# Optimization experiments

Hardware: AMD Instinct MI355X
Metric: run time of the kernel (lower is better)

The kernel has to match this reference:

```python
import jax, jax.numpy as jnp
import numpy as np

BASE_TEMP = 0.07
CLASS_TEMPS = jnp.array([0.08, 0.05, 0.10], dtype=jnp.float32)  # idx 0,1,2
EPS = 1e-08


def setup_inputs() -> dict:
    key = jax.random.key(0)
    k1, k2 = jax.random.split(key)
    B, D = 8192, 128
    embeddings = jax.random.normal(k1, (B, D), dtype=jnp.float32)
    labels = jax.random.randint(k2, (B,), 0, 3, dtype=jnp.int64)
    return {"embeddings": embeddings, "labels": labels}


def reference(embeddings, labels):
    B = embeddings.shape[0]
    # per-row temperature from the row's class label
    temps = CLASS_TEMPS[labels]  # [B]
    sim = jnp.matmul(embeddings, embeddings.T)  # [B, B]
    logits = sim / temps[:, None]
    # subtract detached row max (stability, gradient-stopped as in .detach())
    logits = logits - jax.lax.stop_gradient(jnp.max(logits, axis=1, keepdims=True))
    # denominator includes the self term (original sums exp over all j)
    log_prob = logits - jnp.log(jnp.sum(jnp.exp(logits), axis=1, keepdims=True) + EPS)
    # positives: same label, excluding self
    pos_mask = (labels[:, None] == labels[None, :]).astype(jnp.float32)
    pos_mask = pos_mask * (1.0 - jnp.eye(B, dtype=jnp.float32))
    pos_count = jnp.sum(pos_mask, axis=1)  # [B]
    valid = pos_count > 0
    loss_i = -(BASE_TEMP / temps) * jnp.sum(pos_mask * log_prob, axis=1) / (pos_count + EPS)
    n_valid = jnp.sum(valid.astype(jnp.float32))
    total = jnp.sum(jnp.where(valid, loss_i, 0.0))
    return jnp.where(n_valid > 0, total / jnp.maximum(n_valid, 1.0), 0.0)
```

## Files before the change

### kernel.cpp

```cpp
#include <hip/hip_runtime.h>
#include <hip/hip_bf16.h>


#define B_ROWS 8192
#define D_DIM 128
#define NSPLIT 16
#define JRANGE (B_ROWS / NSPLIT)
#define NSTEPS (JRANGE / 32)
#define BASE_TEMP 0.07f
#define LOG2E 1.4426950408889634f
#define LN2 0.6931471805599453f
#define FIX_SCALE 1048576.0f

typedef __bf16 bf16x8 __attribute__((ext_vector_type(8)));
typedef __bf16 bf16x4 __attribute__((ext_vector_type(4)));
typedef float floatx16 __attribute__((ext_vector_type(16)));
typedef unsigned long long u64;

__device__ __forceinline__ float class_invtemp(int lbl) {
    return (lbl == 0) ? 12.5f : ((lbl == 1) ? 20.0f : 10.0f);
}

__device__ __forceinline__ u64 fix64(float v) {
    return (u64)(long long)llrintf(v * FIX_SCALE);
}

__device__ __forceinline__ void load_lds16(const __bf16* g, __bf16* l) {
    __builtin_amdgcn_global_load_lds(
        (const __attribute__((address_space(1))) void*)g,
        (__attribute__((address_space(3))) void*)l,
        16, 0, 0);
}

__global__ __launch_bounds__(256) void k0_prep(
        const float* __restrict__ E, const int* __restrict__ labels,
        __bf16* __restrict__ Ebf, __bf16* __restrict__ Ebs,
        float* __restrict__ nrm,
        float* __restrict__ Spart ,
        int* __restrict__ cntpart ) {
    const int blk = blockIdx.x;
    const int tid = threadIdx.x;
    const int row0 = blk * 32;

    __shared__ float4 red[3][256];
    __shared__ int scnt[3];
    if (tid < 3) scnt[tid] = 0;

    float4 cls0 = {0.f, 0.f, 0.f, 0.f};
    float4 cls1 = {0.f, 0.f, 0.f, 0.f};
    float4 cls2 = {0.f, 0.f, 0.f, 0.f};

    const float4* src = reinterpret_cast<const float4*>(E + (size_t)row0 * D_DIM);
    #pragma unroll
    for (int p = 0; p < 4; ++p) {
        int idx = p * 256 + tid;
        float4 v = src[idx];
        int r = idx >> 5, k4 = idx & 31;
        int R = row0 + r;
        int lab = labels[R];
        float sc = class_invtemp(lab) * LOG2E;
        int T = R >> 5;
        int l = (R & 31) + ((k4 >> 1) & 1) * 32;
        int c = k4 >> 2;
        size_t dst = (size_t)T * 4096 + c * 512 + l * 8 + (k4 & 1) * 4;
        bf16x4 o  = { (__bf16)v.x, (__bf16)v.y, (__bf16)v.z, (__bf16)v.w };
        bf16x4 os = { (__bf16)(v.x * sc), (__bf16)(v.y * sc),
                      (__bf16)(v.z * sc), (__bf16)(v.w * sc) };
        *reinterpret_cast<bf16x4*>(Ebf + dst) = o;
        *reinterpret_cast<bf16x4*>(Ebs + dst) = os;
        float s = v.x * v.x + v.y * v.y + v.z * v.z + v.w * v.w;
        s += __shfl_xor(s, 1);  s += __shfl_xor(s, 2);  s += __shfl_xor(s, 4);
        s += __shfl_xor(s, 8);  s += __shfl_xor(s, 16);
        if ((tid & 31) == 0) nrm[R] = s;
        if (lab == 0) { cls0.x += v.x; cls0.y += v.y; cls0.z += v.z; cls0.w += v.w; }
        else if (lab == 1) { cls1.x += v.x; cls1.y += v.y; cls1.z += v.z; cls1.w += v.w; }
        else { cls2.x += v.x; cls2.y += v.y; cls2.z += v.z; cls2.w += v.w; }
    }
    red[0][tid] = cls0;
    red[1][tid] = cls1;
    red[2][tid] = cls2;
    if (tid < 32) atomicAdd(&scnt[labels[row0 + tid]], 1);
    __syncthreads();

    if (tid < 128) {
        const int k4 = tid >> 2, comp = tid & 3;
        const float* rf = reinterpret_cast<const float*>(red);
        #pragma unroll
        for (int c = 0; c < 3; ++c) {
            float a = 0.f;
            #pragma unroll
            for (int w = 0; w < 8; ++w)
                a += rf[(c * 256 + k4 + 32 * w) * 4 + comp];
            Spart[((size_t)blk * 3 + c) * 128 + tid] = a;
        }
    }
    if (tid < 3) cntpart[blk * 4 + tid] = scnt[tid];
}

__global__ __launch_bounds__(256) void k2_stats(
        const __bf16* __restrict__ Ebf, const __bf16* __restrict__ Ebs,
        const int* __restrict__ labels, const float* __restrict__ nrm,
        float* __restrict__ part ,
        const float* __restrict__ Spart, const int* __restrict__ cntpart,
        float* __restrict__ S , float* __restrict__ counts ,
        u64* __restrict__ lossfix, u64* __restrict__ validfix,
        unsigned int* __restrict__ done) {
    __shared__ __bf16 Ab[3][4096];

    const int tid = threadIdx.x;
    const int lane = tid & 63;
    const int wave = tid >> 6;
    const int itile = blockIdx.x;
    const int split = blockIdx.y;
    const int col = lane & 31;
    const int icol = itile * 128 + wave * 32 + col;

    const float negm = -class_invtemp(labels[icol]) * LOG2E * nrm[icol];

    const int iT = itile * 4 + wave;
    const __bf16* bbase = Ebs + (size_t)iT * 4096 + lane * 8;
    bf16x8 Bf[8];
    #pragma unroll
    for (int c = 0; c < 8; ++c)
        Bf[c] = *reinterpret_cast<const bf16x8*>(bbase + c * 512);

    floatx16 init0;
    #pragma unroll
    for (int r = 0; r < 16; ++r) init0[r] = negm;

    const __bf16* abase = Ebf + (size_t)split * NSTEPS * 4096;
    const int woff = wave * 1024 + lane * 8;

    load_lds16(abase + woff,              &Ab[0][wave * 1024]);
    load_lds16(abase + woff + 512,        &Ab[0][wave * 1024 + 512]);
    load_lds16(abase + 4096 + woff,       &Ab[1][wave * 1024]);
    load_lds16(abase + 4096 + woff + 512, &Ab[1][wave * 1024 + 512]);

    float Zacc[4];
    #pragma unroll
    for (int q = 0; q < 4; ++q) Zacc[q] = 0.f;

    #pragma unroll 1
    for (int s = 0; s < NSTEPS; ++s) {
        if (s < NSTEPS - 1) {
            asm volatile("s_waitcnt vmcnt(2)" ::: "memory");
        } else {
            asm volatile("s_waitcnt vmcnt(0)" ::: "memory");
        }
        __builtin_amdgcn_s_barrier();
        __builtin_amdgcn_sched_barrier(0);

        if (s + 2 < NSTEPS) {
            const __bf16* g = abase + (size_t)(s + 2) * 4096 + woff;
            __bf16* l = &Ab[(s + 2) % 3][wave * 1024];
            load_lds16(g, l);
            load_lds16(g + 512, l + 512);
        }

        const __bf16* abuf = &Ab[s % 3][0];
        bf16x8 A[8];
        #pragma unroll
        for (int c = 0; c < 8; ++c)
            A[c] = *reinterpret_cast<const bf16x8*>(abuf + c * 512 + lane * 8);

        floatx16 a1;
        #pragma unroll
        for (int r = 0; r < 16; ++r) a1[r] = 0.f;
        floatx16 a0 = __builtin_amdgcn_mfma_f32_32x32x16_bf16(A[0], Bf[0], init0, 0, 0, 0);
        a1 = __builtin_amdgcn_mfma_f32_32x32x16_bf16(A[4], Bf[4], a1, 0, 0, 0);
        a0 = __builtin_amdgcn_mfma_f32_32x32x16_bf16(A[1], Bf[1], a0, 0, 0, 0);
        a1 = __builtin_amdgcn_mfma_f32_32x32x16_bf16(A[5], Bf[5], a1, 0, 0, 0);
        a0 = __builtin_amdgcn_mfma_f32_32x32x16_bf16(A[2], Bf[2], a0, 0, 0, 0);
        a1 = __builtin_amdgcn_mfma_f32_32x32x16_bf16(A[6], Bf[6], a1, 0, 0, 0);
        a0 = __builtin_amdgcn_mfma_f32_32x32x16_bf16(A[3], Bf[3], a0, 0, 0, 0);
        a1 = __builtin_amdgcn_mfma_f32_32x32x16_bf16(A[7], Bf[7], a1, 0, 0, 0);

        #pragma unroll
        for (int q = 0; q < 4; ++q) {
            Zacc[q] += (__builtin_amdgcn_exp2f(a0[4 * q]     + a1[4 * q])
                      + __builtin_amdgcn_exp2f(a0[4 * q + 1] + a1[4 * q + 1]))
                     + (__builtin_amdgcn_exp2f(a0[4 * q + 2] + a1[4 * q + 2])
                      + __builtin_amdgcn_exp2f(a0[4 * q + 3] + a1[4 * q + 3]));
        }
    }

    float Zt = (Zacc[0] + Zacc[1]) + (Zacc[2] + Zacc[3]);
    Zt += __shfl_xor(Zt, 32);
    if (lane < 32)
        part[(size_t)split * B_ROWS + icol] = Zt;

    if (split == 0) {
        if (itile < 3 && tid < 128) {
            float a = 0.f;
            #pragma unroll 8
            for (int g = 0; g < 256; ++g)
                a += Spart[((size_t)g * 3 + itile) * 128 + tid];
            S[itile * 128 + tid] = a;
        } else if (itile == 3 && tid < 3) {
            int a = 0;
            #pragma unroll 8
            for (int g = 0; g < 256; ++g) a += cntpart[g * 4 + tid];
            counts[tid] = (float)a;
        } else if (itile == 4 && tid == 0) {
            *lossfix = 0ull;
            *validfix = 0ull;
            *done = 0u;
        }
    }
}

__global__ __launch_bounds__(256) void k3_rowloss(
        const float* __restrict__ E, const int* __restrict__ labels,
        const float* __restrict__ S, const float* __restrict__ counts,
        const float* __restrict__ nrm, const float* __restrict__ part,
        u64* __restrict__ lossfix, u64* __restrict__ validfix,
        unsigned int* __restrict__ done, float* __restrict__ out) {
    __shared__ float sS[384];
    const int tid = threadIdx.x;
    if (tid < 128) {
        sS[tid]       = S[tid];
        sS[128 + tid] = S[128 + tid];
        sS[256 + tid] = S[256 + tid];
    }
    __syncthreads();

    const int r = tid >> 3, g = tid & 7;
    const int i = blockIdx.x * 32 + r;
    const int lab = labels[i];
    const float invt = class_invtemp(lab);

    const float4* er = reinterpret_cast<const float4*>(E + (size_t)i * D_DIM);
    const float4* sr = reinterpret_cast<const float4*>(&sS[lab * 128]);
    float dotS = 0.f;
    #pragma unroll
    for (int q = 0; q < 4; ++q) {
        float4 v = er[g * 4 + q];
        float4 s = sr[g * 4 + q];
        dotS += v.x * s.x + v.y * s.y + v.z * s.z + v.w * s.w;
    }
    float Zp = 0.f;
    #pragma unroll
    for (int p = 0; p < NSPLIT / 8; ++p)
        Zp += part[(size_t)(g + p * 8) * B_ROWS + i];

    #pragma unroll
    for (int off = 1; off < 8; off <<= 1) {
        dotS += __shfl_xor(dotS, off);
        Zp   += __shfl_xor(Zp, off);
    }

    float loss = 0.f;
    int valid = 0;
    if (g == 0) {
        const float nr = nrm[i];
        const float C = counts[lab] - 1.0f;
        const float lse = invt * nr + LN2 * __builtin_amdgcn_logf(Zp);
        const float P_nat = invt * (dotS - nr);
        if (C > 0.f) {
            loss = -(BASE_TEMP * invt) * (P_nat - C * lse) / (C + 1e-8f);
            valid = 1;
        }
    }
    loss += __shfl_down(loss, 8);   valid += __shfl_down(valid, 8);
    loss += __shfl_down(loss, 16);  valid += __shfl_down(valid, 16);
    loss += __shfl_down(loss, 32);  valid += __shfl_down(valid, 32);

    __shared__ float rl[4];
    __shared__ int rv[4];
    if ((tid & 63) == 0) { rl[tid >> 6] = loss; rv[tid >> 6] = valid; }
    __syncthreads();
    if (tid == 0) {
        float bt = (rl[0] + rl[1]) + (rl[2] + rl[3]);
        int bv = (rv[0] + rv[1]) + (rv[2] + rv[3]);
        atomicAdd(lossfix, fix64(bt));
        atomicAdd(validfix, (u64)bv);
        __threadfence();
        unsigned int t = atomicAdd(done, 1u);
        if (t == gridDim.x - 1) {
            u64 L = atomicAdd(lossfix, 0ull);
            u64 V = atomicAdd(validfix, 0ull);
            double T = (double)(long long)L * (1.0 / (double)FIX_SCALE);
            double N = (double)(long long)V;
            out[0] = (N > 0.0) ? (float)(T / fmax(N, 1.0)) : 0.f;
        }
    }
}

extern "C" void kernel_launch(void* const* d_in, const int* in_sizes, int n_in,
                              void* d_out, int out_size, void* d_ws, size_t ws_size,
                              hipStream_t stream) {
    const float* E = (const float*)d_in[0];
    const int* labels = (const int*)d_in[1];
    float* out = (float*)d_out;
    char* ws = (char*)d_ws;

    const size_t OFF_EBF   = 0;
    const size_t OFF_EBS   = (size_t)2 << 20;
    const size_t OFF_NRM   = (size_t)4 << 20;
    const size_t OFF_SPART = OFF_NRM + 32768;
    const size_t OFF_CNTP  = OFF_SPART + 393216;
    const size_t OFF_S     = OFF_CNTP + 4096;
    const size_t OFF_MISC  = OFF_S + 2048;
    const size_t OFF_PART  = (size_t)5 << 20;

    __bf16* Ebf = (__bf16*)(ws + OFF_EBF);
    __bf16* Ebs = (__bf16*)(ws + OFF_EBS);
    float* nrm = (float*)(ws + OFF_NRM);
    float* Spart = (float*)(ws + OFF_SPART);
    int* cntpart = (int*)(ws + OFF_CNTP);
    float* S = (float*)(ws + OFF_S);
    float* counts = (float*)(ws + OFF_MISC);
    u64* lossfix = (u64*)(ws + OFF_MISC + 16);
    u64* validfix = (u64*)(ws + OFF_MISC + 24);
    unsigned int* done = (unsigned int*)(ws + OFF_MISC + 32);
    float* part = (float*)(ws + OFF_PART);

    k0_prep<<<256, 256, 0, stream>>>(E, labels, Ebf, Ebs, nrm, Spart, cntpart);
    k2_stats<<<dim3(64, NSPLIT), 256, 0, stream>>>(
        Ebf, Ebs, labels, nrm, part, Spart, cntpart, S, counts,
        lossfix, validfix, done);
    k3_rowloss<<<256, 256, 0, stream>>>(E, labels, S, counts, nrm, part,
                                        lossfix, validfix, done, out);
}
```

Before: 47.62 us.

## Software-pipeline MFMA and exp across tiles with double accumulators

Restructures the main loop so each tile's MFMA chain runs while the exp2 reduction of the previous tile's accumulator is computed, using two ping-pong accumulators and a manually unrolled loop with prologue and epilogue. It replaces the two interleaved MFMA chains with one serial chain of eight, adds the max offset at exp time instead of seeding the accumulator, and raises wave priority around the MFMAs with s_setprio. The aim is to hide transcendental and MFMA latency behind each other. The cost is more accumulator registers and a longer dependent MFMA chain.

```diff
diff --git a/kernel.cpp b/kernel.cpp
--- a/kernel.cpp
+++ b/kernel.cpp
@@ -124,10 +124,6 @@
     for (int c = 0; c < 8; ++c)
         Bf[c] = *reinterpret_cast<const bf16x8*>(bbase + c * 512);
 
-    floatx16 init0;
-    #pragma unroll
-    for (int r = 0; r < 16; ++r) init0[r] = negm;
-
     const __bf16* abase = Ebf + (size_t)split * NSTEPS * 4096;
     const int woff = wave * 1024 + lane * 8;
 
@@ -140,48 +136,59 @@
     #pragma unroll
     for (int q = 0; q < 4; ++q) Zacc[q] = 0.f;
 
-    #pragma unroll 1
-    for (int s = 0; s < NSTEPS; ++s) {
-        if (s < NSTEPS - 1) {
-            asm volatile("s_waitcnt vmcnt(2)" ::: "memory");
-        } else {
-            asm volatile("s_waitcnt vmcnt(0)" ::: "memory");
-        }
+    floatx16 accA, accB;
+
+    auto tile_body = [&](int t, floatx16& cur, floatx16& prev,
+                         bool doExp, bool last) {
+        if (!last) asm volatile("s_waitcnt vmcnt(2)" ::: "memory");
+        else       asm volatile("s_waitcnt vmcnt(0)" ::: "memory");
         __builtin_amdgcn_s_barrier();
-        __builtin_amdgcn_sched_barrier(0);
-
-        if (s + 2 < NSTEPS) {
-            const __bf16* g = abase + (size_t)(s + 2) * 4096 + woff;
-            __bf16* l = &Ab[(s + 2) % 3][wave * 1024];
+
+        if (t + 2 < NSTEPS) {
+            const __bf16* g = abase + (size_t)(t + 2) * 4096 + woff;
+            __bf16* l = &Ab[(t + 2) % 3][wave * 1024];
             load_lds16(g, l);
             load_lds16(g + 512, l + 512);
         }
 
-        const __bf16* abuf = &Ab[s % 3][0];
+        const __bf16* abuf = &Ab[t % 3][0];
         bf16x8 A[8];
         #pragma unroll
         for (int c = 0; c < 8; ++c)
             A[c] = *reinterpret_cast<const bf16x8*>(abuf + c * 512 + lane * 8);
 
-        floatx16 a1;
         #pragma unroll
-        for (int r = 0; r < 16; ++r) a1[r] = 0.f;
-        floatx16 a0 = __builtin_amdgcn_mfma_f32_32x32x16_bf16(A[0], Bf[0], init0, 0, 0, 0);
-        a1 = __builtin_amdgcn_mfma_f32_32x32x16_bf16(A[4], Bf[4], a1, 0, 0, 0);
-        a0 = __builtin_amdgcn_mfma_f32_32x32x16_bf16(A[1], Bf[1], a0, 0, 0, 0);
-        a1 = __builtin_amdgcn_mfma_f32_32x32x16_bf16(A[5], Bf[5], a1, 0, 0, 0);
-        a0 = __builtin_amdgcn_mfma_f32_32x32x16_bf16(A[2], Bf[2], a0, 0, 0, 0);
-        a1 = __builtin_amdgcn_mfma_f32_32x32x16_bf16(A[6], Bf[6], a1, 0, 0, 0);
-        a0 = __builtin_amdgcn_mfma_f32_32x32x16_bf16(A[3], Bf[3], a0, 0, 0, 0);
-        a1 = __builtin_amdgcn_mfma_f32_32x32x16_bf16(A[7], Bf[7], a1, 0, 0, 0);
-
+        for (int r = 0; r < 16; ++r) cur[r] = 0.f;
+        __builtin_amdgcn_s_setprio(1);
         #pragma unroll
-        for (int q = 0; q < 4; ++q) {
-            Zacc[q] += (__builtin_amdgcn_exp2f(a0[4 * q]     + a1[4 * q])
-                      + __builtin_amdgcn_exp2f(a0[4 * q + 1] + a1[4 * q + 1]))
-                     + (__builtin_amdgcn_exp2f(a0[4 * q + 2] + a1[4 * q + 2])
-                      + __builtin_amdgcn_exp2f(a0[4 * q + 3] + a1[4 * q + 3]));
-        }
+        for (int c = 0; c < 8; ++c)
+            cur = __builtin_amdgcn_mfma_f32_32x32x16_bf16(A[c], Bf[c], cur, 0, 0, 0);
+        __builtin_amdgcn_s_setprio(0);
+
+        if (doExp) {
+            #pragma unroll
+            for (int q = 0; q < 4; ++q) {
+                Zacc[q] += (__builtin_amdgcn_exp2f(prev[4 * q]     + negm)
+                          + __builtin_amdgcn_exp2f(prev[4 * q + 1] + negm))
+                         + (__builtin_amdgcn_exp2f(prev[4 * q + 2] + negm)
+                          + __builtin_amdgcn_exp2f(prev[4 * q + 3] + negm));
+            }
+        }
+    };
+
+    tile_body(0, accA, accB, false, false);
+    #pragma unroll 1
+    for (int t = 1; t <= NSTEPS - 3; t += 2) {
+        tile_body(t,     accB, accA, true, false);
+        tile_body(t + 1, accA, accB, true, false);
+    }
+    tile_body(NSTEPS - 1, accB, accA, true, true);
+    #pragma unroll
+    for (int q = 0; q < 4; ++q) {
+        Zacc[q] += (__builtin_amdgcn_exp2f(accB[4 * q]     + negm)
+                  + __builtin_amdgcn_exp2f(accB[4 * q + 1] + negm))
+                 + (__builtin_amdgcn_exp2f(accB[4 * q + 2] + negm)
+                  + __builtin_amdgcn_exp2f(accB[4 * q + 3] + negm));
     }
 
     float Zt = (Zacc[0] + Zacc[1]) + (Zacc[2] + Zacc[3]);
```

Measured after the change: 47.10 us. About the same (-1.1%).

## Process two column tiles per iteration with four-slot LDS ring and one barrier

Applied to the files above, without the earlier changes.

The stats loop now handles two 32-column steps per iteration. It uses a 4-deep LDS ring instead of 3, issues both prefetches together, and waits for loads and syncs only once per pair. Each step gets its own full-K accumulator chain, interleaved so the two chains can overlap. The max-shift is added before exp2 instead of being seeded into the MFMA accumulator. The aim is to halve barrier and waitcnt overhead, at the cost of more LDS per block and a full vmcnt(0) drain each interval.

```diff
diff --git a/kernel.cpp b/kernel.cpp
--- a/kernel.cpp
+++ b/kernel.cpp
@@ -7,6 +7,7 @@
 #define NSPLIT 16
 #define JRANGE (B_ROWS / NSPLIT)
 #define NSTEPS (JRANGE / 32)
+#define NINTERVALS (NSTEPS / 2)
 #define BASE_TEMP 0.07f
 #define LOG2E 1.4426950408889634f
 #define LN2 0.6931471805599453f
@@ -105,7 +106,7 @@
         float* __restrict__ S , float* __restrict__ counts ,
         u64* __restrict__ lossfix, u64* __restrict__ validfix,
         unsigned int* __restrict__ done) {
-    __shared__ __bf16 Ab[3][4096];
+    __shared__ __bf16 Ab[4][4096];
 
     const int tid = threadIdx.x;
     const int lane = tid & 63;
@@ -124,10 +125,6 @@
     for (int c = 0; c < 8; ++c)
         Bf[c] = *reinterpret_cast<const bf16x8*>(bbase + c * 512);
 
-    floatx16 init0;
-    #pragma unroll
-    for (int r = 0; r < 16; ++r) init0[r] = negm;
-
     const __bf16* abase = Ebf + (size_t)split * NSTEPS * 4096;
     const int woff = wave * 1024 + lane * 8;
 
@@ -141,46 +138,66 @@
     for (int q = 0; q < 4; ++q) Zacc[q] = 0.f;
 
     #pragma unroll 1
-    for (int s = 0; s < NSTEPS; ++s) {
-        if (s < NSTEPS - 1) {
-            asm volatile("s_waitcnt vmcnt(2)" ::: "memory");
-        } else {
-            asm volatile("s_waitcnt vmcnt(0)" ::: "memory");
-        }
+    for (int iv = 0; iv < NINTERVALS; ++iv) {
+        const int t0 = 2 * iv, t1 = 2 * iv + 1;
+
+        asm volatile("s_waitcnt vmcnt(0)" ::: "memory");
         __builtin_amdgcn_s_barrier();
-        __builtin_amdgcn_sched_barrier(0);
-
-        if (s + 2 < NSTEPS) {
-            const __bf16* g = abase + (size_t)(s + 2) * 4096 + woff;
-            __bf16* l = &Ab[(s + 2) % 3][wave * 1024];
-            load_lds16(g, l);
-            load_lds16(g + 512, l + 512);
-        }
-
-        const __bf16* abuf = &Ab[s % 3][0];
-        bf16x8 A[8];
+
+        if (t0 + 2 < NSTEPS) {
+            const __bf16* g0 = abase + (size_t)(t0 + 2) * 4096 + woff;
+            __bf16* l0 = &Ab[(t0 + 2) & 3][wave * 1024];
+            load_lds16(g0, l0);
+            load_lds16(g0 + 512, l0 + 512);
+            const __bf16* g1 = abase + (size_t)(t1 + 2) * 4096 + woff;
+            __bf16* l1 = &Ab[(t1 + 2) & 3][wave * 1024];
+            load_lds16(g1, l1);
+            load_lds16(g1 + 512, l1 + 512);
+        }
+
+        const __bf16* b0 = &Ab[t0 & 3][0];
+        const __bf16* b1 = &Ab[t1 & 3][0];
+
+        floatx16 acc0, acc1;
         #pragma unroll
-        for (int c = 0; c < 8; ++c)
-            A[c] = *reinterpret_cast<const bf16x8*>(abuf + c * 512 + lane * 8);
-
-        floatx16 a1;
-        #pragma unroll
-        for (int r = 0; r < 16; ++r) a1[r] = 0.f;
-        floatx16 a0 = __builtin_amdgcn_mfma_f32_32x32x16_bf16(A[0], Bf[0], init0, 0, 0, 0);
-        a1 = __builtin_amdgcn_mfma_f32_32x32x16_bf16(A[4], Bf[4], a1, 0, 0, 0);
-        a0 = __builtin_amdgcn_mfma_f32_32x32x16_bf16(A[1], Bf[1], a0, 0, 0, 0);
-        a1 = __builtin_amdgcn_mfma_f32_32x32x16_bf16(A[5], Bf[5], a1, 0, 0, 0);
-        a0 = __builtin_amdgcn_mfma_f32_32x32x16_bf16(A[2], Bf[2], a0, 0, 0, 0);
-        a1 = __builtin_amdgcn_mfma_f32_32x32x16_bf16(A[6], Bf[6], a1, 0, 0, 0);
-        a0 = __builtin_amdgcn_mfma_f32_32x32x16_bf16(A[3], Bf[3], a0, 0, 0, 0);
-        a1 = __builtin_amdgcn_mfma_f32_32x32x16_bf16(A[7], Bf[7], a1, 0, 0, 0);
+        for (int r = 0; r < 16; ++r) { acc0[r] = 0.f; acc1[r] = 0.f; }
+        {
+            bf16x8 A0[4], A1[4];
+            #pragma unroll
+            for (int c = 0; c < 4; ++c) {
+                A0[c] = *reinterpret_cast<const bf16x8*>(b0 + c * 512 + lane * 8);
+                A1[c] = *reinterpret_cast<const bf16x8*>(b1 + c * 512 + lane * 8);
+            }
+            #pragma unroll
+            for (int c = 0; c < 4; ++c) {
+                acc0 = __builtin_amdgcn_mfma_f32_32x32x16_bf16(A0[c], Bf[c], acc0, 0, 0, 0);
+                acc1 = __builtin_amdgcn_mfma_f32_32x32x16_bf16(A1[c], Bf[c], acc1, 0, 0, 0);
+            }
+        }
+        {
+            bf16x8 A0[4], A1[4];
+            #pragma unroll
+            for (int c = 0; c < 4; ++c) {
+                A0[c] = *reinterpret_cast<const bf16x8*>(b0 + (c + 4) * 512 + lane * 8);
+                A1[c] = *reinterpret_cast<const bf16x8*>(b1 + (c + 4) * 512 + lane * 8);
+            }
+            #pragma unroll
+            for (int c = 0; c < 4; ++c) {
+                acc0 = __builtin_amdgcn_mfma_f32_32x32x16_bf16(A0[c], Bf[c + 4], acc0, 0, 0, 0);
+                acc1 = __builtin_amdgcn_mfma_f32_32x32x16_bf16(A1[c], Bf[c + 4], acc1, 0, 0, 0);
+            }
+        }
 
         #pragma unroll
         for (int q = 0; q < 4; ++q) {
-            Zacc[q] += (__builtin_amdgcn_exp2f(a0[4 * q]     + a1[4 * q])
-                      + __builtin_amdgcn_exp2f(a0[4 * q + 1] + a1[4 * q + 1]))
-                     + (__builtin_amdgcn_exp2f(a0[4 * q + 2] + a1[4 * q + 2])
-                      + __builtin_amdgcn_exp2f(a0[4 * q + 3] + a1[4 * q + 3]));
+            Zacc[q] += (__builtin_amdgcn_exp2f(acc0[4 * q]     + negm)
+                      + __builtin_amdgcn_exp2f(acc0[4 * q + 1] + negm))
+                     + (__builtin_amdgcn_exp2f(acc0[4 * q + 2] + negm)
+                      + __builtin_amdgcn_exp2f(acc0[4 * q + 3] + negm));
+            Zacc[q] += (__builtin_amdgcn_exp2f(acc1[4 * q]     + negm)
+                      + __builtin_amdgcn_exp2f(acc1[4 * q + 1] + negm))
+                     + (__builtin_amdgcn_exp2f(acc1[4 * q + 2] + negm)
+                      + __builtin_amdgcn_exp2f(acc1[4 * q + 3] + negm));
         }
     }
 
```

New measurement: 46.33 us. 2.7% less time.
